# Performance work log

Hardware: AMD Instinct MI355X
Metric: run time of the kernel (lower is better)

The kernel has to match this reference:

```python
import jax, jax.numpy as jnp
import numpy as np

U, S, D = 4096, 8192, 32
NUM_REGIONS = 128
GA = 0.1


def setup_inputs() -> dict:
    key = jax.random.key(0)
    k1, k2, k3, k4, k5, k6 = jax.random.split(key, 6)
    user_emb = jax.random.normal(k1, (U, D), dtype=jnp.float32) * 0.01
    item_emb = jax.random.normal(k2, (S, D), dtype=jnp.float32) * 0.01
    train_mask = jax.random.randint(k3, (U, S), 0, 2, dtype=jnp.int32)
    true_qos = jax.random.normal(k4, (U, S), dtype=jnp.float32)
    us_lossweight = jax.random.uniform(k5, (U, S), dtype=jnp.float32)
    region_index = jax.random.randint(k6, (U,), 0, NUM_REGIONS, dtype=jnp.int32)
    return {
        "user_emb": user_emb,
        "item_emb": item_emb,
        "train_mask": train_mask,
        "true_qos": true_qos,
        "us_lossweight": us_lossweight,
        "region_index": region_index,
    }


def _region_loss(user_emb, region_index):
    # per-region sums and counts via a single segment reduction
    sums = jax.ops.segment_sum(user_emb, region_index, num_segments=NUM_REGIONS)  # [R, D]
    counts = jax.ops.segment_sum(jnp.ones((user_emb.shape[0],), dtype=user_emb.dtype),
                                 region_index, num_segments=NUM_REGIONS)  # [R]
    cnt = counts[region_index]                      # [U]
    loo_mean = (sums[region_index] - user_emb) / jnp.maximum(cnt - 1.0, 1.0)[:, None]
    dev = jnp.abs(user_emb - loo_mean)              # [U, D]
    # regions with a single user are skipped in the original loop
    valid = (cnt > 1.0)[:, None]
    return jnp.sum(jnp.where(valid, dev, 0.0))


def reference(user_emb, item_emb, train_mask, true_qos, us_lossweight, region_index):
    pre_qos = (user_emb @ item_emb.T) * train_mask.astype(user_emb.dtype)  # [U, S]
    mse = (pre_qos - true_qos) ** 2
    loss = jnp.sum(us_lossweight * mse)
    regionloss = _region_loss(user_emb, region_index)
    return loss + GA * regionloss
```

## Files before the change

### kernel.cpp

```cpp
#include <hip/hip_runtime.h>

#define U 4096
#define S 8192
#define D 32
#define NUM_REGIONS 128
#define GA 0.1f

#define TU 32
#define TI 512
#define THREADS 256


__global__ void region_accum_kernel(const float* __restrict__ user_emb,
                                    const int* __restrict__ region_index,
                                    float* __restrict__ sums,
                                    float* __restrict__ counts) {
    int idx = blockIdx.x * blockDim.x + threadIdx.x;
    if (idx >= U * D) return;
    int u = idx >> 5;
    int d = idx & (D - 1);
    int r = region_index[u];
    atomicAdd(&sums[r * D + d], user_emb[idx]);
    if (d == 0) atomicAdd(&counts[r], 1.0f);
}

__global__ void region_loss_kernel(const float* __restrict__ user_emb,
                                   const int* __restrict__ region_index,
                                   const float* __restrict__ sums,
                                   const float* __restrict__ counts,
                                   float* __restrict__ rl_accum) {
    int idx = blockIdx.x * blockDim.x + threadIdx.x;
    float v = 0.0f;
    if (idx < U * D) {
        int u = idx >> 5;
        int d = idx & (D - 1);
        int r = region_index[u];
        float cnt = counts[r];
        if (cnt > 1.0f) {
            float e = user_emb[idx];
            float loo = (sums[r * D + d] - e) / fmaxf(cnt - 1.0f, 1.0f);
            v = fabsf(e - loo);
        }
    }
    #pragma unroll
    for (int off = 32; off > 0; off >>= 1) v += __shfl_down(v, off, 64);
    __shared__ float wp[THREADS / 64];
    int lane = threadIdx.x & 63, wid = threadIdx.x >> 6;
    if (lane == 0) wp[wid] = v;
    __syncthreads();
    if (threadIdx.x == 0) {
        float t = 0.0f;
        #pragma unroll
        for (int i = 0; i < THREADS / 64; i++) t += wp[i];
        atomicAdd(rl_accum, t);
    }
}


__global__ __launch_bounds__(THREADS) void mse_kernel(
    const float* __restrict__ user_emb,
    const float* __restrict__ item_emb,
    const int* __restrict__ train_mask,
    const float* __restrict__ true_qos,
    const float* __restrict__ us_lossweight,
    float* __restrict__ loss_accum) {
    __shared__ float uemb[TU][D];

    const int ub = blockIdx.x * TU;
    const int sb = blockIdx.y * TI;

    {
        const float4* src = (const float4*)(user_emb + (size_t)ub * D);
        ((float4*)&uemb[0][0])[threadIdx.x] = src[threadIdx.x];
    }
    __syncthreads();

    const int s0 = sb + 2 * threadIdx.x;

    float4 ir0[8], ir1[8];
    {
        const float4* ip0 = (const float4*)(item_emb + (size_t)s0 * D);
        const float4* ip1 = (const float4*)(item_emb + (size_t)(s0 + 1) * D);
        #pragma unroll
        for (int k = 0; k < 8; k++) { ir0[k] = ip0[k]; ir1[k] = ip1[k]; }
    }

    float acc = 0.0f;
    #pragma unroll 1
    for (int uu = 0; uu < TU; uu++) {
        const size_t base = (size_t)(ub + uu) * S + s0;
        int2   m = *(const int2*)(train_mask + base);
        float2 q = *(const float2*)(true_qos + base);
        float2 w = *(const float2*)(us_lossweight + base);

        float d0 = 0.0f, d1 = 0.0f;
        const float4* ur = (const float4*)&uemb[uu][0];
        #pragma unroll
        for (int k = 0; k < 8; k++) {
            float4 uv = ur[k];
            d0 += uv.x * ir0[k].x + uv.y * ir0[k].y + uv.z * ir0[k].z + uv.w * ir0[k].w;
            d1 += uv.x * ir1[k].x + uv.y * ir1[k].y + uv.z * ir1[k].z + uv.w * ir1[k].w;
        }
        float p0 = d0 * (float)m.x;
        float p1 = d1 * (float)m.y;
        float e0 = p0 - q.x;
        float e1 = p1 - q.y;
        acc += w.x * e0 * e0 + w.y * e1 * e1;
    }

    #pragma unroll
    for (int off = 32; off > 0; off >>= 1) acc += __shfl_down(acc, off, 64);
    __shared__ float wp[THREADS / 64];
    int lane = threadIdx.x & 63, wid = threadIdx.x >> 6;
    if (lane == 0) wp[wid] = acc;
    __syncthreads();
    if (threadIdx.x == 0) {
        float t = 0.0f;
        #pragma unroll
        for (int i = 0; i < THREADS / 64; i++) t += wp[i];
        atomicAdd(loss_accum, t);
    }
}

__global__ void finalize_kernel(const float* __restrict__ loss_acc,
                                const float* __restrict__ rl_acc,
                                float* __restrict__ out) {
    out[0] = loss_acc[0] + GA * rl_acc[0];
}

extern "C" void kernel_launch(void* const* d_in, const int* in_sizes, int n_in,
                              void* d_out, int out_size, void* d_ws, size_t ws_size,
                              hipStream_t stream) {
    const float* user_emb      = (const float*)d_in[0];
    const float* item_emb      = (const float*)d_in[1];
    const int*   train_mask    = (const int*)d_in[2];
    const float* true_qos      = (const float*)d_in[3];
    const float* us_lossweight = (const float*)d_in[4];
    const int*   region_index  = (const int*)d_in[5];
    float* out = (float*)d_out;

    float* ws       = (float*)d_ws;
    float* sums     = ws;
    float* counts   = sums + NUM_REGIONS * D;
    float* loss_acc = counts + NUM_REGIONS;
    float* rl_acc   = loss_acc + 1;
    size_t zero_bytes = (size_t)(NUM_REGIONS * D + NUM_REGIONS + 2) * sizeof(float);
    hipMemsetAsync(d_ws, 0, zero_bytes, stream);

    region_accum_kernel<<<(U * D + 255) / 256, 256, 0, stream>>>(
        user_emb, region_index, sums, counts);
    region_loss_kernel<<<(U * D + 255) / 256, 256, 0, stream>>>(
        user_emb, region_index, sums, counts, rl_acc);

    dim3 grid(U / TU, S / TI);
    mse_kernel<<<grid, THREADS, 0, stream>>>(
        user_emb, item_emb, train_mask, true_qos, us_lossweight, loss_acc);

    finalize_kernel<<<1, 1, 0, stream>>>(loss_acc, rl_acc, out);
}
```

Baseline: 401.4 us.

## Fuse region loss into one block, prefetch mse loads, finalize via last-block counter

Replaces the memset, two region kernels and the finalize kernel with a single-block region kernel that accumulates sums and counts in LDS, then writes the region loss and zeroes the accumulators. The mse kernel now software-prefetches the next row's mask, qos and weight before computing the current row. It finishes with a done-counter so the last block writes the final output. This removes three launches and global atomics. The cost is that the region work runs serially on one workgroup (131k LDS atomics) ahead of the mse kernel.

```diff
diff --git a/kernel.cpp b/kernel.cpp
--- a/kernel.cpp
+++ b/kernel.cpp
@@ -9,50 +9,58 @@
 #define TU 32
 #define TI 512
 #define THREADS 256
+#define GRID_X (U / TU)
+#define GRID_Y (S / TI)
+#define NBLOCKS (GRID_X * GRID_Y)
 
 
-__global__ void region_accum_kernel(const float* __restrict__ user_emb,
-                                    const int* __restrict__ region_index,
-                                    float* __restrict__ sums,
-                                    float* __restrict__ counts) {
-    int idx = blockIdx.x * blockDim.x + threadIdx.x;
-    if (idx >= U * D) return;
-    int u = idx >> 5;
-    int d = idx & (D - 1);
-    int r = region_index[u];
-    atomicAdd(&sums[r * D + d], user_emb[idx]);
-    if (d == 0) atomicAdd(&counts[r], 1.0f);
-}
+__global__ __launch_bounds__(1024) void region_kernel(
+    const float* __restrict__ user_emb,
+    const int* __restrict__ region_index,
+    float* __restrict__ rl_acc,
+    float* __restrict__ loss_acc,
+    unsigned int* __restrict__ done_counter) {
+    __shared__ float sum_lds[NUM_REGIONS * D];
+    __shared__ float cnt_lds[NUM_REGIONS];
+    __shared__ float wred[16];
 
-__global__ void region_loss_kernel(const float* __restrict__ user_emb,
-                                   const int* __restrict__ region_index,
-                                   const float* __restrict__ sums,
-                                   const float* __restrict__ counts,
-                                   float* __restrict__ rl_accum) {
-    int idx = blockIdx.x * blockDim.x + threadIdx.x;
-    float v = 0.0f;
-    if (idx < U * D) {
-        int u = idx >> 5;
-        int d = idx & (D - 1);
+    const int tid = threadIdx.x;
+
+    for (int i = tid; i < NUM_REGIONS * D; i += 1024) sum_lds[i] = 0.0f;
+    if (tid < NUM_REGIONS) cnt_lds[tid] = 0.0f;
+    __syncthreads();
+
+    for (int u = tid; u < U; u += 1024)
+        atomicAdd(&cnt_lds[region_index[u]], 1.0f);
+    for (int idx = tid; idx < U * D; idx += 1024) {
+        int u = idx >> 5, d = idx & (D - 1);
+        atomicAdd(&sum_lds[region_index[u] * D + d], user_emb[idx]);
+    }
+    __syncthreads();
+
+    float local = 0.0f;
+    for (int idx = tid; idx < U * D; idx += 1024) {
+        int u = idx >> 5, d = idx & (D - 1);
         int r = region_index[u];
-        float cnt = counts[r];
-        if (cnt > 1.0f) {
+        float c = cnt_lds[r];
+        if (c > 1.0f) {
             float e = user_emb[idx];
-            float loo = (sums[r * D + d] - e) / fmaxf(cnt - 1.0f, 1.0f);
-            v = fabsf(e - loo);
+            float loo = (sum_lds[r * D + d] - e) / fmaxf(c - 1.0f, 1.0f);
+            local += fabsf(e - loo);
         }
     }
     #pragma unroll
-    for (int off = 32; off > 0; off >>= 1) v += __shfl_down(v, off, 64);
-    __shared__ float wp[THREADS / 64];
-    int lane = threadIdx.x & 63, wid = threadIdx.x >> 6;
-    if (lane == 0) wp[wid] = v;
+    for (int off = 32; off > 0; off >>= 1) local += __shfl_down(local, off, 64);
+    int lane = tid & 63, wid = tid >> 6;
+    if (lane == 0) wred[wid] = local;
     __syncthreads();
-    if (threadIdx.x == 0) {
+    if (tid == 0) {
         float t = 0.0f;
         #pragma unroll
-        for (int i = 0; i < THREADS / 64; i++) t += wp[i];
-        atomicAdd(rl_accum, t);
+        for (int i = 0; i < 16; i++) t += wred[i];
+        rl_acc[0] = t;
+        loss_acc[0] = 0.0f;
+        done_counter[0] = 0u;
     }
 }
 
@@ -63,7 +71,10 @@
     const int* __restrict__ train_mask,
     const float* __restrict__ true_qos,
     const float* __restrict__ us_lossweight,
-    float* __restrict__ loss_accum) {
+    float* __restrict__ loss_acc,
+    const float* __restrict__ rl_acc,
+    unsigned int* __restrict__ done_counter,
+    float* __restrict__ out) {
     __shared__ float uemb[TU][D];
 
     const int ub = blockIdx.x * TU;
@@ -85,13 +96,18 @@
         for (int k = 0; k < 8; k++) { ir0[k] = ip0[k]; ir1[k] = ip1[k]; }
     }
 
+    size_t base = (size_t)ub * S + s0;
+    int2   m = *(const int2*)(train_mask + base);
+    float2 q = *(const float2*)(true_qos + base);
+    float2 w = *(const float2*)(us_lossweight + base);
+
     float acc = 0.0f;
     #pragma unroll 1
     for (int uu = 0; uu < TU; uu++) {
-        const size_t base = (size_t)(ub + uu) * S + s0;
-        int2   m = *(const int2*)(train_mask + base);
-        float2 q = *(const float2*)(true_qos + base);
-        float2 w = *(const float2*)(us_lossweight + base);
+        size_t nbase = base + (uu < TU - 1 ? (size_t)S : 0);
+        int2   mn = *(const int2*)(train_mask + nbase);
+        float2 qn = *(const float2*)(true_qos + nbase);
+        float2 wn = *(const float2*)(us_lossweight + nbase);
 
         float d0 = 0.0f, d1 = 0.0f;
         const float4* ur = (const float4*)&uemb[uu][0];
@@ -106,6 +122,8 @@
         float e0 = p0 - q.x;
         float e1 = p1 - q.y;
         acc += w.x * e0 * e0 + w.y * e1 * e1;
+
+        m = mn; q = qn; w = wn; base = nbase;
     }
 
     #pragma unroll
@@ -118,14 +136,15 @@
         float t = 0.0f;
         #pragma unroll
         for (int i = 0; i < THREADS / 64; i++) t += wp[i];
-        atomicAdd(loss_accum, t);
+        atomicAdd(loss_acc, t);
+        __threadfence();
+        unsigned int n = atomicAdd(done_counter, 1u);
+        if (n == NBLOCKS - 1) {
+            float total = atomicAdd(loss_acc, 0.0f);
+            float rl    = atomicAdd((float*)rl_acc, 0.0f);
+            out[0] = total + GA * rl;
+        }
     }
-}
-
-__global__ void finalize_kernel(const float* __restrict__ loss_acc,
-                                const float* __restrict__ rl_acc,
-                                float* __restrict__ out) {
-    out[0] = loss_acc[0] + GA * rl_acc[0];
 }
 
 extern "C" void kernel_launch(void* const* d_in, const int* in_sizes, int n_in,
@@ -139,22 +158,16 @@
     const int*   region_index  = (const int*)d_in[5];
     float* out = (float*)d_out;
 
-    float* ws       = (float*)d_ws;
-    float* sums     = ws;
-    float* counts   = sums + NUM_REGIONS * D;
-    float* loss_acc = counts + NUM_REGIONS;
-    float* rl_acc   = loss_acc + 1;
-    size_t zero_bytes = (size_t)(NUM_REGIONS * D + NUM_REGIONS + 2) * sizeof(float);
-    hipMemsetAsync(d_ws, 0, zero_bytes, stream);
+    float* ws            = (float*)d_ws;
+    float* rl_acc        = ws;
+    float* loss_acc      = ws + 1;
+    unsigned int* done_counter = (unsigned int*)(ws + 2);
 
-    region_accum_kernel<<<(U * D + 255) / 256, 256, 0, stream>>>(
-        user_emb, region_index, sums, counts);
-    region_loss_kernel<<<(U * D + 255) / 256, 256, 0, stream>>>(
-        user_emb, region_index, sums, counts, rl_acc);
+    region_kernel<<<1, 1024, 0, stream>>>(user_emb, region_index,
+                                          rl_acc, loss_acc, done_counter);
 
-    dim3 grid(U / TU, S / TI);
+    dim3 grid(GRID_X, GRID_Y);
     mse_kernel<<<grid, THREADS, 0, stream>>>(
-        user_emb, item_emb, train_mask, true_qos, us_lossweight, loss_acc);
-
-    finalize_kernel<<<1, 1, 0, stream>>>(loss_acc, rl_acc, out);
+        user_emb, item_emb, train_mask, true_qos, us_lossweight,
+        loss_acc, rl_acc, done_counter, out);
 }
```

Result: slower. 664.2 us (+65.5%).
